# Kernel optimization log

Hardware: AMD Instinct MI355X
Metric: run time of the kernel (lower is better)

## Reference

```python
import jax, jax.numpy as jnp
import numpy as np

NUM_HEAD = 8


def setup_inputs() -> dict:
    key = jax.random.key(0)
    k1, k2, k3 = jax.random.split(key, 3)
    B, C, H, W = 8, 512, 32, 32
    x = jax.random.normal(k1, (B, C, H, W), dtype=jnp.float32)
    # 1x1 conv weights stored as plain matrices (out_ch, in_ch)
    Wqkv = jax.random.normal(k2, (3 * C, C), dtype=jnp.float32) * (1.0 / np.sqrt(C))
    Wo = jax.random.normal(k3, (C, C), dtype=jnp.float32) * (1.0 / np.sqrt(C))
    bo = jnp.zeros((C,), dtype=jnp.float32)
    return {"x": x, "Wqkv": Wqkv, "Wo": Wo, "bo": bo}


def reference(x, Wqkv, Wo, bo):
    B, C, H, W = x.shape
    nh = NUM_HEAD
    d = C // nh
    S = H * W
    scale = 1.0 / np.sqrt(d)
    # 1x1 conv == channel matmul: (B,3C,H,W)
    x_ = jnp.einsum('bchw,oc->bohw', x, Wqkv)
    # reshape to (B, nh, 3d, H, W) and chunk along dim 2 (matches torch chunk order)
    qkv = x_.reshape(B, nh, 3 * d, H, W)
    q, k, v = qkv[:, :, :d], qkv[:, :, d:2 * d], qkv[:, :, 2 * d:]
    # flatten heads into batch, spatial into sequence
    q = q.reshape(B * nh, d, S).transpose(0, 2, 1) * scale  # (BH, S, d)
    k = k.reshape(B * nh, d, S)                             # (BH, d, S)
    v = v.reshape(B * nh, d, S).transpose(0, 2, 1)          # (BH, S, d)
    attn = jax.nn.softmax(jnp.matmul(q, k), axis=-1)        # (BH, S, S)
    out = jnp.matmul(attn, v)                               # (BH, S, d)
    result = out.transpose(0, 2, 1).reshape(B, C, H, W)
    # output 1x1 conv with bias + residual
    y = jnp.einsum('bchw,oc->bohw', result, Wo) + bo[None, :, None, None]
    return y + x
```

## Files before the change

kernel.cpp:

```cpp
#include <hip/hip_runtime.h>
#include <hip/hip_bf16.h>

#define C_DIM 512
#define S_DIM 1024
#define NH 8
#define HD 64

typedef __attribute__((ext_vector_type(8))) short bf16x8;
typedef __attribute__((ext_vector_type(8))) unsigned short u16x8;
typedef __attribute__((ext_vector_type(4))) unsigned short u16x4;
typedef __attribute__((ext_vector_type(4))) float f32x4;

__device__ __forceinline__ unsigned short f2b_hw(float f) {
  __hip_bfloat16 h = __float2bfloat16(f);
  return __builtin_bit_cast(unsigned short, h);
}

__device__ __forceinline__ f32x4 mfma16(bf16x8 a, bf16x8 b, f32x4 c) {
  return __builtin_amdgcn_mfma_f32_16x16x32_bf16(a, b, c, 0, 0, 0);
}

__device__ __forceinline__ void gload_lds16(const unsigned short* g, unsigned short* l) {
  __builtin_amdgcn_global_load_lds(
      (const __attribute__((address_space(1))) unsigned int*)g,
      (__attribute__((address_space(3))) unsigned int*)l, 16, 0, 0);
}

__global__ __launch_bounds__(256) void prep(
    const float* __restrict__ x, const float* __restrict__ Wqkv,
    const float* __restrict__ Wo,
    unsigned short* __restrict__ WqkvB, unsigned short* __restrict__ WoB,
    unsigned short* __restrict__ xT)
{
  __shared__ float T[64][65];
  const int bid = blockIdx.x;
  if (bid < 1024) {
    const int i = bid * 256 + threadIdx.x;
    const float* src;
    unsigned short* dst;
    int off;
    float mul = 1.0f;
    if (i < 196608) {
      src = Wqkv; dst = WqkvB; off = i * 4;
      const int o = off >> 9;
      if ((o % 192) < 64) mul = 0.18033688011112042f;
    } else {
      src = Wo; dst = WoB; off = (i - 196608) * 4;
    }
    const float4 v = *(const float4*)(src + off);
    const u16x4 pk = {f2b_hw(v.x * mul), f2b_hw(v.y * mul),
                      f2b_hw(v.z * mul), f2b_hw(v.w * mul)};
    *(u16x4*)(dst + off) = pk;
  } else {
    const int idx = bid - 1024;
    const int st = idx & 15, ct = (idx >> 4) & 7, b = idx >> 7;
    const int c0 = ct * 64, s0 = st * 64;
    const int tr = threadIdx.x >> 4, tc4 = (threadIdx.x & 15) * 4;
#pragma unroll
    for (int rep = 0; rep < 4; ++rep) {
      const int c = rep * 16 + tr;
      *(float4*)&T[c][tc4] =
          *(const float4*)(x + ((size_t)(b * C_DIM + c0 + c)) * S_DIM + s0 + tc4);
    }
    __syncthreads();
#pragma unroll
    for (int rep = 0; rep < 4; ++rep) {
      const int s = rep * 16 + tr;
      const u16x4 pk = {f2b_hw(T[tc4 + 0][s]), f2b_hw(T[tc4 + 1][s]),
                        f2b_hw(T[tc4 + 2][s]), f2b_hw(T[tc4 + 3][s])};
      *(u16x4*)(xT + ((size_t)(b * S_DIM + s0 + s)) * C_DIM + c0 + tc4) = pk;
    }
  }
}

template <int MODE>
__global__ __launch_bounds__(256) void mfma_proj(
    const unsigned short* __restrict__ A, const unsigned short* __restrict__ Bm,
    unsigned short* __restrict__ Q, unsigned short* __restrict__ K,
    unsigned short* __restrict__ Vt,
    float* __restrict__ y, const float* __restrict__ bo,
    const float* __restrict__ resid)
{
  const int b = blockIdx.z, ot = blockIdx.y, st = blockIdx.x;
  const int o0 = ot * 128, s0 = st * 128;
  const int tid = threadIdx.x;
  const int w = tid >> 6, lane = tid & 63;
  const int g = lane >> 4, j16 = lane & 15;
  const int wr = w >> 1, wc = w & 1;

  __shared__ __align__(16) unsigned short lds[2048 * 8];
  char* const Al = (char*)lds;
  char* const Bl = (char*)lds + 16384;

  f32x4 acc[4][4];
#pragma unroll
  for (int mt = 0; mt < 4; ++mt)
#pragma unroll
    for (int nt = 0; nt < 4; ++nt) {
      acc[mt][nt].x = 0.f; acc[mt][nt].y = 0.f;
      acc[mt][nt].z = 0.f; acc[mt][nt].w = 0.f;
    }

  for (int k0 = 0; k0 < C_DIM; k0 += 64) {
    __syncthreads();
#pragma unroll
    for (int it = 0; it < 8; ++it) {
      const int chunk = it * 256 + tid;
      const int cid = chunk & 1023;
      const int row = cid >> 3;
      const int colb = (cid & 7) << 4;
      const int srcb = colb ^ ((row & 7) << 4);
      const unsigned short* gp;
      if (it < 4) gp = A + (size_t)(o0 + row) * C_DIM + k0 + (srcb >> 1);
      else        gp = Bm + ((size_t)(b * S_DIM) + s0 + row) * C_DIM + k0 + (srcb >> 1);
      gload_lds16(gp, lds + (size_t)(it * 256 + w * 64) * 8);
    }
    __syncthreads();

#pragma unroll
    for (int ks = 0; ks < 2; ++ks) {
      bf16x8 af[4], bfr[4];
#pragma unroll
      for (int mt = 0; mt < 4; ++mt) {
        const int r = wr * 64 + mt * 16 + j16;
        af[mt] = __builtin_bit_cast(
            bf16x8, *(const u16x8*)(Al + r * 128 + ((ks * 64 + g * 16) ^ ((r & 7) << 4))));
      }
#pragma unroll
      for (int nt = 0; nt < 4; ++nt) {
        const int r = wc * 64 + nt * 16 + j16;
        bfr[nt] = __builtin_bit_cast(
            bf16x8, *(const u16x8*)(Bl + r * 128 + ((ks * 64 + g * 16) ^ ((r & 7) << 4))));
      }
#pragma unroll
      for (int mt = 0; mt < 4; ++mt)
#pragma unroll
        for (int nt = 0; nt < 4; ++nt)
          acc[mt][nt] = mfma16(af[mt], bfr[nt], acc[mt][nt]);
    }
  }

#pragma unroll
  for (int mt = 0; mt < 4; ++mt) {
    const int ob = o0 + wr * 64 + mt * 16 + g * 4;
    if (MODE == 0) {
      const int head = ob / 192, type = (ob % 192) >> 6, d = ob & 63;
      const int bh = b * NH + head;
      if (type < 2) {
        unsigned short* const dst = (type == 0) ? Q : K;
#pragma unroll
        for (int nt = 0; nt < 4; ++nt) {
          const int s = s0 + wc * 64 + nt * 16 + j16;
          const f32x4 a = acc[mt][nt];
          const u16x4 pk = {f2b_hw(a.x), f2b_hw(a.y), f2b_hw(a.z), f2b_hw(a.w)};
          *(u16x4*)(dst + ((size_t)bh * S_DIM + s) * HD + d) = pk;
        }
      } else {
#pragma unroll
        for (int nt = 0; nt < 4; ++nt) {
          const int spos = nt * 16 + j16;
          const int p = (spos & 35) | ((spos & 12) << 1) | ((spos & 16) >> 2);
          const size_t col = (size_t)(s0 + wc * 64 + p);
          const f32x4 a = acc[mt][nt];
#pragma unroll
          for (int q = 0; q < 4; ++q)
            Vt[((size_t)bh * HD + d + q) * S_DIM + col] = f2b_hw(a[q]);
        }
      }
    } else {
#pragma unroll
      for (int nt = 0; nt < 4; ++nt) {
        const int s = s0 + wc * 64 + nt * 16 + j16;
#pragma unroll
        for (int q = 0; q < 4; ++q) {
          const int o = ob + q;
          const size_t idx = ((size_t)(b * C_DIM + o)) * S_DIM + s;
          y[idx] = acc[mt][nt][q] + bo[o] + resid[idx];
        }
      }
    }
  }
}

__global__ __launch_bounds__(512) void attn_mfma(
    const unsigned short* __restrict__ Qg, const unsigned short* __restrict__ Kg,
    const unsigned short* __restrict__ Vg, unsigned short* __restrict__ AOt)
{
  const int bh = blockIdx.x;
  const int qb = blockIdx.y;
  const int b = bh >> 3, head = bh & 7;
  const int tid = threadIdx.x;
  const int w = tid >> 6, lane = tid & 63;
  const int g = lane >> 4, j16 = lane & 15;
  const int qw0 = qb * 256 + w * 32;

  __shared__ __align__(16) unsigned short KV[3][2][4096];

  bf16x8 qf[2][2];
#pragma unroll
  for (int nt = 0; nt < 2; ++nt)
#pragma unroll
    for (int ks = 0; ks < 2; ++ks)
      qf[nt][ks] = __builtin_bit_cast(
          bf16x8, *(const u16x8*)(Qg + ((size_t)bh * S_DIM + qw0 + nt * 16 + j16) * HD +
                                  ks * 32 + g * 8));

  auto STAGE = [&](int buf, int k0) {
    const int cid = tid;
    const int row = cid >> 3;
    const int srcb = ((cid & 7) << 4) ^ ((row & 7) << 4);
    unsigned short* const dst = &KV[buf][0][0] + (size_t)(w * 64) * 8;
    gload_lds16(Kg + ((size_t)bh * S_DIM + k0 + row) * HD + (srcb >> 1), dst);
    gload_lds16(Vg + ((size_t)bh * HD + row) * S_DIM + k0 + (srcb >> 1), dst + 4096);
  };

  f32x4 oacc[4][2];
#pragma unroll
  for (int mt = 0; mt < 4; ++mt)
#pragma unroll
    for (int nt = 0; nt < 2; ++nt) {
      oacc[mt][nt].x = 0.f; oacc[mt][nt].y = 0.f;
      oacc[mt][nt].z = 0.f; oacc[mt][nt].w = 0.f;
    }
  float lsum[2] = {0.f, 0.f};

  STAGE(0, 0);
  STAGE(1, 64);

  for (int kt = 0; kt < 16; ++kt) {
    if (kt < 15) asm volatile("s_waitcnt vmcnt(2)" ::: "memory");
    else         asm volatile("s_waitcnt vmcnt(0)" ::: "memory");
    __builtin_amdgcn_s_barrier();
    if (kt < 14) STAGE((kt + 2) % 3, (kt + 2) * 64);

    const char* const Kl = (const char*)KV + (kt % 3) * 16384;
    const char* const Vl = Kl + 8192;

    f32x4 sacc[4][2];
    __builtin_amdgcn_s_setprio(1);
#pragma unroll
    for (int mt = 0; mt < 4; ++mt) {
      const int row = mt * 16 + j16;
      const int sw = (row & 7) << 4;
      const bf16x8 kf0 = __builtin_bit_cast(
          bf16x8, *(const u16x8*)(Kl + row * 128 + ((g * 16) ^ sw)));
#pragma unroll
      for (int nt = 0; nt < 2; ++nt) {
        f32x4 z; z.x = 0.f; z.y = 0.f; z.z = 0.f; z.w = 0.f;
        sacc[mt][nt] = mfma16(kf0, qf[nt][0], z);
      }
      const bf16x8 kf1 = __builtin_bit_cast(
          bf16x8, *(const u16x8*)(Kl + row * 128 + ((64 + g * 16) ^ sw)));
#pragma unroll
      for (int nt = 0; nt < 2; ++nt)
        sacc[mt][nt] = mfma16(kf1, qf[nt][1], sacc[mt][nt]);
    }
    __builtin_amdgcn_s_setprio(0);

    u16x4 pf4[2][4];
#pragma unroll
    for (int mt = 0; mt < 4; ++mt)
#pragma unroll
      for (int nt = 0; nt < 2; ++nt) {
        f32x4 p;
        p.x = exp2f(sacc[mt][nt].x);
        p.y = exp2f(sacc[mt][nt].y);
        p.z = exp2f(sacc[mt][nt].z);
        p.w = exp2f(sacc[mt][nt].w);
        lsum[nt] += (p.x + p.y) + (p.z + p.w);
        pf4[nt][mt] = u16x4{f2b_hw(p.x), f2b_hw(p.y), f2b_hw(p.z), f2b_hw(p.w)};
      }

    __builtin_amdgcn_s_setprio(1);
#pragma unroll
    for (int ks = 0; ks < 2; ++ks) {
      bf16x8 pfr[2];
#pragma unroll
      for (int nt = 0; nt < 2; ++nt)
        pfr[nt] = __builtin_bit_cast(
            bf16x8, __builtin_shufflevector(pf4[nt][2 * ks], pf4[nt][2 * ks + 1],
                                            0, 1, 2, 3, 4, 5, 6, 7));
#pragma unroll
      for (int mt = 0; mt < 4; ++mt) {
        const int row = mt * 16 + j16;
        const int sw = (row & 7) << 4;
        const bf16x8 vf = __builtin_bit_cast(
            bf16x8, *(const u16x8*)(Vl + row * 128 + ((ks * 64 + g * 16) ^ sw)));
#pragma unroll
        for (int nt = 0; nt < 2; ++nt)
          oacc[mt][nt] = mfma16(vf, pfr[nt], oacc[mt][nt]);
      }
    }
    __builtin_amdgcn_s_setprio(0);
  }

#pragma unroll
  for (int nt = 0; nt < 2; ++nt) {
    lsum[nt] += __shfl_xor(lsum[nt], 16);
    lsum[nt] += __shfl_xor(lsum[nt], 32);
    lsum[nt] = 1.f / lsum[nt];
  }

#pragma unroll
  for (int mt = 0; mt < 4; ++mt)
#pragma unroll
    for (int nt = 0; nt < 2; ++nt) {
      const int q = qw0 + nt * 16 + j16;
      const f32x4 a = oacc[mt][nt];
      const float rl = lsum[nt];
      const u16x4 pk = {f2b_hw(a.x * rl), f2b_hw(a.y * rl), f2b_hw(a.z * rl), f2b_hw(a.w * rl)};
      *(u16x4*)(AOt + ((size_t)(b * S_DIM + q)) * C_DIM + head * HD + mt * 16 + g * 4) = pk;
    }
}

extern "C" void kernel_launch(void* const* d_in, const int* in_sizes, int n_in,
                              void* d_out, int out_size, void* d_ws, size_t ws_size,
                              hipStream_t stream) {
  const float* x    = (const float*)d_in[0];
  const float* Wqkv = (const float*)d_in[1];
  const float* Wo   = (const float*)d_in[2];
  const float* bo   = (const float*)d_in[3];
  float* y = (float*)d_out;

  unsigned short* WqkvB = (unsigned short*)d_ws;
  unsigned short* WoB   = WqkvB + 786432;
  unsigned short* xT    = WoB + 262144;
  unsigned short* Q     = xT + 4194304;
  unsigned short* K     = Q + 4194304;
  unsigned short* Vt    = K + 4194304;
  unsigned short* AOt   = Vt + 4194304;

  prep<<<dim3(2048), 256, 0, stream>>>(x, Wqkv, Wo, WqkvB, WoB, xT);
  mfma_proj<0><<<dim3(8, 12, 8), 256, 0, stream>>>(WqkvB, xT, Q, K, Vt,
                                                   nullptr, nullptr, nullptr);
  attn_mfma<<<dim3(64, 4), 512, 0, stream>>>(Q, K, Vt, AOt);
  mfma_proj<1><<<dim3(8, 4, 8), 256, 0, stream>>>(WoB, AOt, nullptr, nullptr, nullptr,
                                                  y, bo, x);
}
```

Before: 81.89 us.

## Use 256-thread attention blocks with 128-key double-buffered KV tiles

Attention blocks shrink from 8 waves to 4 waves (128 queries each), and the grid doubles to 512 blocks. The KV staging moves from a 3-deep ring of 64-key tiles with vmcnt waits to a 2-deep double buffer of 128-key tiles, each processed in two 64-key sub-steps, with V using a 16-row XOR swizzle. The aim is to halve the number of barrier and wait rounds and improve occupancy and load balance across CUs. In exchange, the __syncthreads right after issuing loads leaves less prefetch overlap, and each block reloads K/V for fewer queries, which doubles total KV traffic.

```diff
diff --git a/kernel.cpp b/kernel.cpp
--- a/kernel.cpp
+++ b/kernel.cpp
@@ -182,7 +182,7 @@
   }
 }
 
-__global__ __launch_bounds__(512) void attn_mfma(
+__global__ __launch_bounds__(256) void attn_mfma(
     const unsigned short* __restrict__ Qg, const unsigned short* __restrict__ Kg,
     const unsigned short* __restrict__ Vg, unsigned short* __restrict__ AOt)
 {
@@ -192,9 +192,9 @@
   const int tid = threadIdx.x;
   const int w = tid >> 6, lane = tid & 63;
   const int g = lane >> 4, j16 = lane & 15;
-  const int qw0 = qb * 256 + w * 32;
-
-  __shared__ __align__(16) unsigned short KV[3][2][4096];
+  const int qw0 = qb * 128 + w * 32;
+
+  __shared__ __align__(16) unsigned short KV[2][2][8192];
 
   bf16x8 qf[2][2];
 #pragma unroll
@@ -206,12 +206,20 @@
                                   ks * 32 + g * 8));
 
   auto STAGE = [&](int buf, int k0) {
-    const int cid = tid;
-    const int row = cid >> 3;
-    const int srcb = ((cid & 7) << 4) ^ ((row & 7) << 4);
-    unsigned short* const dst = &KV[buf][0][0] + (size_t)(w * 64) * 8;
-    gload_lds16(Kg + ((size_t)bh * S_DIM + k0 + row) * HD + (srcb >> 1), dst);
-    gload_lds16(Vg + ((size_t)bh * HD + row) * S_DIM + k0 + (srcb >> 1), dst + 4096);
+    unsigned short* const Kd = &KV[buf][0][0];
+    unsigned short* const Vd = &KV[buf][1][0];
+#pragma unroll
+    for (int it = 0; it < 4; ++it) {
+      const int cid = it * 256 + tid;
+      const int krow = cid >> 3;
+      const int ksrc = ((cid & 7) << 4) ^ ((krow & 7) << 4);
+      gload_lds16(Kg + ((size_t)bh * S_DIM + k0 + krow) * HD + (ksrc >> 1),
+                  Kd + (size_t)(it * 256 + w * 64) * 8);
+      const int vrow = cid >> 4;
+      const int vsrc = ((cid & 15) << 4) ^ ((vrow & 15) << 4);
+      gload_lds16(Vg + ((size_t)bh * HD + vrow) * S_DIM + k0 + (vsrc >> 1),
+                  Vd + (size_t)(it * 256 + w * 64) * 8);
+    }
   };
 
   f32x4 oacc[4][2];
@@ -225,73 +233,74 @@
   float lsum[2] = {0.f, 0.f};
 
   STAGE(0, 0);
-  STAGE(1, 64);
-
-  for (int kt = 0; kt < 16; ++kt) {
-    if (kt < 15) asm volatile("s_waitcnt vmcnt(2)" ::: "memory");
-    else         asm volatile("s_waitcnt vmcnt(0)" ::: "memory");
-    __builtin_amdgcn_s_barrier();
-    if (kt < 14) STAGE((kt + 2) % 3, (kt + 2) * 64);
-
-    const char* const Kl = (const char*)KV + (kt % 3) * 16384;
-    const char* const Vl = Kl + 8192;
-
-    f32x4 sacc[4][2];
-    __builtin_amdgcn_s_setprio(1);
-#pragma unroll
-    for (int mt = 0; mt < 4; ++mt) {
-      const int row = mt * 16 + j16;
-      const int sw = (row & 7) << 4;
-      const bf16x8 kf0 = __builtin_bit_cast(
-          bf16x8, *(const u16x8*)(Kl + row * 128 + ((g * 16) ^ sw)));
-#pragma unroll
-      for (int nt = 0; nt < 2; ++nt) {
-        f32x4 z; z.x = 0.f; z.y = 0.f; z.z = 0.f; z.w = 0.f;
-        sacc[mt][nt] = mfma16(kf0, qf[nt][0], z);
-      }
-      const bf16x8 kf1 = __builtin_bit_cast(
-          bf16x8, *(const u16x8*)(Kl + row * 128 + ((64 + g * 16) ^ sw)));
-#pragma unroll
-      for (int nt = 0; nt < 2; ++nt)
-        sacc[mt][nt] = mfma16(kf1, qf[nt][1], sacc[mt][nt]);
-    }
-    __builtin_amdgcn_s_setprio(0);
-
-    u16x4 pf4[2][4];
-#pragma unroll
-    for (int mt = 0; mt < 4; ++mt)
-#pragma unroll
-      for (int nt = 0; nt < 2; ++nt) {
-        f32x4 p;
-        p.x = exp2f(sacc[mt][nt].x);
-        p.y = exp2f(sacc[mt][nt].y);
-        p.z = exp2f(sacc[mt][nt].z);
-        p.w = exp2f(sacc[mt][nt].w);
-        lsum[nt] += (p.x + p.y) + (p.z + p.w);
-        pf4[nt][mt] = u16x4{f2b_hw(p.x), f2b_hw(p.y), f2b_hw(p.z), f2b_hw(p.w)};
-      }
-
-    __builtin_amdgcn_s_setprio(1);
-#pragma unroll
-    for (int ks = 0; ks < 2; ++ks) {
-      bf16x8 pfr[2];
-#pragma unroll
-      for (int nt = 0; nt < 2; ++nt)
-        pfr[nt] = __builtin_bit_cast(
-            bf16x8, __builtin_shufflevector(pf4[nt][2 * ks], pf4[nt][2 * ks + 1],
-                                            0, 1, 2, 3, 4, 5, 6, 7));
+
+#pragma unroll
+  for (int kt = 0; kt < 8; ++kt) {
+    __syncthreads();
+    if (kt < 7) STAGE((kt + 1) & 1, (kt + 1) * 128);
+
+    const char* const Kl = (const char*)&KV[kt & 1][0][0];
+    const char* const Vl = (const char*)&KV[kt & 1][1][0];
+
+#pragma unroll
+    for (int sub = 0; sub < 2; ++sub) {
+      f32x4 sacc[4][2];
+      __builtin_amdgcn_s_setprio(1);
 #pragma unroll
       for (int mt = 0; mt < 4; ++mt) {
-        const int row = mt * 16 + j16;
+        const int row = sub * 64 + mt * 16 + j16;
         const int sw = (row & 7) << 4;
-        const bf16x8 vf = __builtin_bit_cast(
-            bf16x8, *(const u16x8*)(Vl + row * 128 + ((ks * 64 + g * 16) ^ sw)));
+        const bf16x8 kf0 = __builtin_bit_cast(
+            bf16x8, *(const u16x8*)(Kl + row * 128 + ((g * 16) ^ sw)));
+#pragma unroll
+        for (int nt = 0; nt < 2; ++nt) {
+          f32x4 z; z.x = 0.f; z.y = 0.f; z.z = 0.f; z.w = 0.f;
+          sacc[mt][nt] = mfma16(kf0, qf[nt][0], z);
+        }
+        const bf16x8 kf1 = __builtin_bit_cast(
+            bf16x8, *(const u16x8*)(Kl + row * 128 + ((64 + g * 16) ^ sw)));
 #pragma unroll
         for (int nt = 0; nt < 2; ++nt)
-          oacc[mt][nt] = mfma16(vf, pfr[nt], oacc[mt][nt]);
-      }
-    }
-    __builtin_amdgcn_s_setprio(0);
+          sacc[mt][nt] = mfma16(kf1, qf[nt][1], sacc[mt][nt]);
+      }
+      __builtin_amdgcn_s_setprio(0);
+
+      u16x4 pf4[2][4];
+#pragma unroll
+      for (int mt = 0; mt < 4; ++mt)
+#pragma unroll
+        for (int nt = 0; nt < 2; ++nt) {
+          f32x4 p;
+          p.x = exp2f(sacc[mt][nt].x);
+          p.y = exp2f(sacc[mt][nt].y);
+          p.z = exp2f(sacc[mt][nt].z);
+          p.w = exp2f(sacc[mt][nt].w);
+          lsum[nt] += (p.x + p.y) + (p.z + p.w);
+          pf4[nt][mt] = u16x4{f2b_hw(p.x), f2b_hw(p.y), f2b_hw(p.z), f2b_hw(p.w)};
+        }
+
+      __builtin_amdgcn_s_setprio(1);
+#pragma unroll
+      for (int ks2 = 0; ks2 < 2; ++ks2) {
+        bf16x8 pfr[2];
+#pragma unroll
+        for (int nt = 0; nt < 2; ++nt)
+          pfr[nt] = __builtin_bit_cast(
+              bf16x8, __builtin_shufflevector(pf4[nt][2 * ks2], pf4[nt][2 * ks2 + 1],
+                                              0, 1, 2, 3, 4, 5, 6, 7));
+#pragma unroll
+        for (int mt = 0; mt < 4; ++mt) {
+          const int vrow = mt * 16 + j16;
+          const int col = (sub * 128 + ks2 * 64 + g * 16) ^ ((vrow & 15) << 4);
+          const bf16x8 vf = __builtin_bit_cast(
+              bf16x8, *(const u16x8*)(Vl + vrow * 256 + col));
+#pragma unroll
+          for (int nt = 0; nt < 2; ++nt)
+            oacc[mt][nt] = mfma16(vf, pfr[nt], oacc[mt][nt]);
+        }
+      }
+      __builtin_amdgcn_s_setprio(0);
+    }
   }
 
 #pragma unroll
@@ -333,7 +342,7 @@
   prep<<<dim3(2048), 256, 0, stream>>>(x, Wqkv, Wo, WqkvB, WoB, xT);
   mfma_proj<0><<<dim3(8, 12, 8), 256, 0, stream>>>(WqkvB, xT, Q, K, Vt,
                                                    nullptr, nullptr, nullptr);
-  attn_mfma<<<dim3(64, 4), 512, 0, stream>>>(Q, K, Vt, AOt);
+  attn_mfma<<<dim3(64, 8), 256, 0, stream>>>(Q, K, Vt, AOt);
   mfma_proj<1><<<dim3(8, 4, 8), 256, 0, stream>>>(WoB, AOt, nullptr, nullptr, nullptr,
                                                   y, bo, x);
 }
```

After: 103.8 us. 26.7% more time.
